# Optimization experiments

Measured on AMD Instinct MI355X. Metric: run time of the kernel, lower is better.

The kernel has to match this reference:

```python
import jax, jax.numpy as jnp
import numpy as np

EPS = 1e-5
NUM_GROUPS = 8


def _group_norm(x, w, b, num_groups, eps=EPS):
    # x: [BN, C, T], normalize per-sample over each group of channels and time
    BN, C, T = x.shape
    xg = x.reshape(BN, num_groups, C // num_groups, T)
    mean = xg.mean(axis=(2, 3), keepdims=True)
    var = xg.var(axis=(2, 3), keepdims=True)
    xg = (xg - mean) * jax.lax.rsqrt(var + eps)
    x = xg.reshape(BN, C, T)
    return x * w[None, :, None] + b[None, :, None]


def _layer_norm(x, w, b, eps=EPS):
    mean = x.mean(axis=-1, keepdims=True)
    var = x.var(axis=-1, keepdims=True)
    return (x - mean) * jax.lax.rsqrt(var + eps) * w + b


def setup_inputs() -> dict:
    key = jax.random.key(0)
    ks = jax.random.split(key, 8)
    B, T, N, C_in, C_out, K, kt = 16, 128, 64, 128, 256, 3, 3
    x = jax.random.normal(ks[0], (B, T, N, C_in), dtype=jnp.float32)
    A = jax.random.uniform(ks[1], (K, N, N), dtype=jnp.float32)
    dw_weights = jax.random.uniform(ks[2], (K, C_in), minval=0.8, maxval=1.2, dtype=jnp.float32)
    W_pw = jax.random.normal(ks[3], (C_out, K * C_in), dtype=jnp.float32) / np.sqrt(K * C_in)
    W_conv = jax.random.normal(ks[4], (C_out, 1, kt), dtype=jnp.float32) / np.sqrt(kt)
    gn_w = jnp.ones((C_out,), dtype=jnp.float32)
    gn_b = jnp.zeros((C_out,), dtype=jnp.float32)
    ln_w = jnp.ones((C_out,), dtype=jnp.float32)
    ln_b = jnp.zeros((C_out,), dtype=jnp.float32)
    W_res = jax.random.normal(ks[5], (C_out, C_in), dtype=jnp.float32) / np.sqrt(C_in)
    return {"x": x, "A": A, "dw_weights": dw_weights, "W_pw": W_pw, "W_conv": W_conv,
            "gn_w": gn_w, "gn_b": gn_b, "ln_w": ln_w, "ln_b": ln_b, "W_res": W_res}


def reference(x, A, dw_weights, W_pw, W_conv, gn_w, gn_b, ln_w, ln_b, W_res):
    B, T, N, C = x.shape
    K = A.shape[0]
    C_out = W_pw.shape[0]
    # residual projection (C_in != C_out)
    residual = jnp.einsum('btnc,oc->btno', x, W_res)
    # NOTE: faithful to torch einsum 'knm,btnc->kbtnc' (sums A over m only)
    agg = jnp.einsum('knm,btnc->kbtnc', A, x)
    agg = agg * dw_weights[:, None, None, None, :]
    # stack K along feature dim: [B,T,N,K*C]
    h = jnp.transpose(agg, (1, 2, 3, 0, 4)).reshape(B, T, N, K * C)
    h = jnp.einsum('btnk,ok->btno', h, W_pw)  # pointwise, no bias; dropout=eval identity
    # depthwise temporal conv over T: [B*N, C_out, T]
    h_t = jnp.transpose(h, (0, 2, 3, 1)).reshape(B * N, C_out, T)
    pad = W_conv.shape[-1] // 2
    h_t = jax.lax.conv_general_dilated(
        h_t, W_conv, window_strides=(1,), padding=[(pad, pad)],
        dimension_numbers=('NCH', 'OIH', 'NCH'), feature_group_count=C_out)
    h_t = _group_norm(h_t, gn_w, gn_b, NUM_GROUPS)
    h = jnp.transpose(h_t.reshape(B, N, C_out, T), (0, 3, 1, 2))
    return jax.nn.gelu(_layer_norm(h + residual, ln_w, ln_b), approximate=False)
```

## Files before the change

kernel.cpp:

```cpp
#include <hip/hip_runtime.h>

typedef unsigned short u16;
typedef __attribute__((ext_vector_type(4))) unsigned short u16x4;
typedef __attribute__((ext_vector_type(8))) __bf16 bf16x8;
typedef __attribute__((ext_vector_type(4))) float f32x4;

#define B_ 16
#define T_ 128
#define N_ 64
#define CI 128
#define CO 256

__device__ __forceinline__ u16 f2b(float f) {
    unsigned x = __builtin_bit_cast(unsigned, f);
    x += 0x7fffu + ((x >> 16) & 1u);
    return (u16)(x >> 16);
}

__global__ void prep_kernel(const float* __restrict__ A, const float* __restrict__ dw,
                            const float* __restrict__ Wpw, const float* __restrict__ Wres,
                            u16* __restrict__ Mg, u16* __restrict__ WresB) {
    int n = blockIdx.x >> 2, ch = blockIdx.x & 3;
    int tid = threadIdx.x;
    float s0 = 0.f, s1 = 0.f, s2 = 0.f;
    for (int m = 0; m < N_; ++m) {
        s0 += A[(0 * N_ + n) * N_ + m];
        s1 += A[(1 * N_ + n) * N_ + m];
        s2 += A[(2 * N_ + n) * N_ + m];
    }
#pragma unroll
    for (int i = 0; i < 8; ++i) {
        int e4 = tid + i * 256;
        int ol = e4 >> 5, c4 = (e4 & 31) << 2;
        int o = ch * 64 + ol;
        float4 d0 = *(const float4*)(dw + c4);
        float4 d1 = *(const float4*)(dw + CI + c4);
        float4 d2 = *(const float4*)(dw + 2 * CI + c4);
        float4 p0 = *(const float4*)(Wpw + (size_t)o * 3 * CI + c4);
        float4 p1 = *(const float4*)(Wpw + (size_t)o * 3 * CI + CI + c4);
        float4 p2 = *(const float4*)(Wpw + (size_t)o * 3 * CI + 2 * CI + c4);
        u16x4 u = { f2b(s0 * d0.x * p0.x + s1 * d1.x * p1.x + s2 * d2.x * p2.x),
                    f2b(s0 * d0.y * p0.y + s1 * d1.y * p1.y + s2 * d2.y * p2.y),
                    f2b(s0 * d0.z * p0.z + s1 * d1.z * p1.z + s2 * d2.z * p2.z),
                    f2b(s0 * d0.w * p0.w + s1 * d1.w * p1.w + s2 * d2.w * p2.w) };
        *(u16x4*)(Mg + ((size_t)n << 15) + o * CI + c4) = u;
        if (n == 0) {
            float4 r = *(const float4*)(Wres + (size_t)o * CI + c4);
            u16x4 ur = { f2b(r.x), f2b(r.y), f2b(r.z), f2b(r.w) };
            *(u16x4*)(WresB + o * CI + c4) = ur;
        }
    }
}

__global__ __launch_bounds__(512, 2) void fused_kernel(
    const float* __restrict__ xg, const u16* __restrict__ Mg, const u16* __restrict__ WresB,
    const float* __restrict__ Wconv, const float* __restrict__ gnw, const float* __restrict__ gnb,
    const float* __restrict__ lnw, const float* __restrict__ lnb, float* __restrict__ out)
{
    __shared__ __align__(16) u16 xf[T_ * CI];
    __shared__ float ebA[CO], ebB[CO];
    __shared__ float gpart[8][2][2];
    __shared__ float gstat[8][2];
    __shared__ float lnp[T_][10];
    __shared__ float lnstat[T_][2];

    const int tid = threadIdx.x;
    const int bid = blockIdx.x;
    const int n = bid & 63, b = bid >> 6;
    const float* xb = xg + (((size_t)b * T_) * N_ + n) * CI;

#pragma unroll
    for (int it = 0; it < 8; ++it) {
        int f = tid + (it << 9);
        int t = f >> 5;
        int c4 = (f & 31) << 2;
        float4 v = *(const float4*)(xb + (size_t)t * (N_ * CI) + c4);
        int kkk = c4 >> 5, quad = (c4 >> 3) & 3, j = c4 & 7;
        int mt = t >> 4;
        int sl = quad * 16 + (t & 15);
        int off = ((kkk * 8 + mt) << 9) + (sl << 3) + j;
        u16x4 u = { f2b(v.x), f2b(v.y), f2b(v.z), f2b(v.w) };
        *(u16x4*)(xf + off) = u;
    }
    __syncthreads();

    const int wid = tid >> 6, lane = tid & 63;
    const int wt = wid >> 2, wo = wid & 3;
    const int lr = lane & 15, lq = lane >> 4;

    f32x4 ah[4][4], ar[4][4];
#pragma unroll
    for (int mi = 0; mi < 4; ++mi)
#pragma unroll
        for (int ni = 0; ni < 4; ++ni) {
            ah[mi][ni] = (f32x4){0.f, 0.f, 0.f, 0.f};
            ar[mi][ni] = (f32x4){0.f, 0.f, 0.f, 0.f};
        }
    const u16* Mn = Mg + ((size_t)n << 15);
#pragma unroll
    for (int kk = 0; kk < 4; ++kk) {
        bf16x8 af[4];
#pragma unroll
        for (int mi = 0; mi < 4; ++mi)
            af[mi] = *(const bf16x8*)(xf + ((kk * 8 + wt * 4 + mi) << 9) + (lane << 3));
        const int c = kk * 32 + lq * 8;
#pragma unroll
        for (int ni = 0; ni < 4; ++ni) {
            const int o = wo * 64 + ni * 16 + lr;
            bf16x8 bm = *(const bf16x8*)(Mn + o * CI + c);
            bf16x8 br = *(const bf16x8*)(WresB + o * CI + c);
#pragma unroll
            for (int mi = 0; mi < 4; ++mi) {
                ah[mi][ni] = __builtin_amdgcn_mfma_f32_16x16x32_bf16(af[mi], bm, ah[mi][ni], 0, 0, 0);
                ar[mi][ni] = __builtin_amdgcn_mfma_f32_16x16x32_bf16(af[mi], br, ar[mi][ni], 0, 0, 0);
            }
        }
    }

    if (wt == 0 && lq == 3) {
#pragma unroll
        for (int ni = 0; ni < 4; ++ni) ebA[wo * 64 + ni * 16 + lr] = ah[3][ni][3];
    }
    if (wt == 1 && lq == 0) {
#pragma unroll
        for (int ni = 0; ni < 4; ++ni) ebB[wo * 64 + ni * 16 + lr] = ah[0][ni][0];
    }
    __syncthreads();

    float w0[4], w1[4], w2[4];
#pragma unroll
    for (int ni = 0; ni < 4; ++ni) {
        int o = wo * 64 + ni * 16 + lr;
        w0[ni] = Wconv[o * 3 + 0];
        w1[ni] = Wconv[o * 3 + 1];
        w2[ni] = Wconv[o * 3 + 2];
    }

    float gs0 = 0.f, gq0 = 0.f, gs1 = 0.f, gq1 = 0.f;
#pragma unroll
    for (int ni = 0; ni < 4; ++ni) {
        int o = wo * 64 + ni * 16 + lr;
        float up3[4], dn0[4];
#pragma unroll
        for (int mi = 0; mi < 4; ++mi) up3[mi] = __shfl(ah[mi][ni][3], (lane + 48) & 63);
#pragma unroll
        for (int mi = 0; mi < 4; ++mi) dn0[mi] = __shfl(ah[mi][ni][0], (lane + 16) & 63);
        float epv = ebA[o], env = ebB[o];
        float sA = 0.f, qA = 0.f;
#pragma unroll
        for (int mi = 0; mi < 4; ++mi) {
            float prev = (lq == 0) ? ((mi == 0) ? ((wt == 1) ? epv : 0.f) : up3[mi - 1]) : up3[mi];
            float nxt3 = (lq == 3) ? ((mi == 3) ? ((wt == 0) ? env : 0.f) : dn0[mi + 1]) : dn0[mi];
            float hm1 = prev;
#pragma unroll
            for (int e = 0; e < 4; ++e) {
                float cur = ah[mi][ni][e];
                float nx = (e < 3) ? ah[mi][ni][e + 1] : nxt3;
                float hc = w0[ni] * hm1 + w1[ni] * cur + w2[ni] * nx;
                hm1 = cur;
                ah[mi][ni][e] = hc;
                sA += hc;
                qA += hc * hc;
            }
        }
        if ((ni >> 1) == 0) { gs0 += sA; gq0 += qA; } else { gs1 += sA; gq1 += qA; }
    }
#pragma unroll
    for (int m = 1; m < 64; m <<= 1) {
        gs0 += __shfl_xor(gs0, m); gq0 += __shfl_xor(gq0, m);
        gs1 += __shfl_xor(gs1, m); gq1 += __shfl_xor(gq1, m);
    }
    if (lane == 0) {
        gpart[wid][0][0] = gs0; gpart[wid][0][1] = gq0;
        gpart[wid][1][0] = gs1; gpart[wid][1][1] = gq1;
    }
    __syncthreads();
    if (tid < 8) {
        float s = gpart[tid >> 1][tid & 1][0] + gpart[(tid >> 1) + 4][tid & 1][0];
        float q = gpart[tid >> 1][tid & 1][1] + gpart[(tid >> 1) + 4][tid & 1][1];
        float mu = s * (1.f / 4096.f);
        float var = q * (1.f / 4096.f) - mu * mu;
        gstat[tid][0] = mu;
        gstat[tid][1] = rsqrtf(var + 1e-5f);
    }
    __syncthreads();

    float lw[4], lb[4];
    float st[4][4], qt[4][4];
#pragma unroll
    for (int mi = 0; mi < 4; ++mi)
#pragma unroll
        for (int e = 0; e < 4; ++e) { st[mi][e] = 0.f; qt[mi][e] = 0.f; }
#pragma unroll
    for (int ni = 0; ni < 4; ++ni) {
        int o = wo * 64 + ni * 16 + lr;
        lw[ni] = lnw[o]; lb[ni] = lnb[o];
        float mg = gstat[wo * 2 + (ni >> 1)][0];
        float rg = gstat[wo * 2 + (ni >> 1)][1];
        float gwm = gnw[o] * rg;
        float gbm = gnb[o] - mg * gwm;
#pragma unroll
        for (int mi = 0; mi < 4; ++mi)
#pragma unroll
            for (int e = 0; e < 4; ++e) {
                float v = ah[mi][ni][e] * gwm + gbm + ar[mi][ni][e];
                ah[mi][ni][e] = v;
                st[mi][e] += v;
                qt[mi][e] += v * v;
            }
    }
#pragma unroll
    for (int m = 1; m < 16; m <<= 1)
#pragma unroll
        for (int mi = 0; mi < 4; ++mi)
#pragma unroll
            for (int e = 0; e < 4; ++e) {
                st[mi][e] += __shfl_xor(st[mi][e], m);
                qt[mi][e] += __shfl_xor(qt[mi][e], m);
            }
    if (lr == 0) {
#pragma unroll
        for (int mi = 0; mi < 4; ++mi)
#pragma unroll
            for (int e = 0; e < 4; ++e) {
                int t = wt * 64 + mi * 16 + lq * 4 + e;
                lnp[t][wo * 2] = st[mi][e];
                lnp[t][wo * 2 + 1] = qt[mi][e];
            }
    }
    __syncthreads();
    if (tid < T_) {
        float s = lnp[tid][0] + lnp[tid][2] + lnp[tid][4] + lnp[tid][6];
        float q = lnp[tid][1] + lnp[tid][3] + lnp[tid][5] + lnp[tid][7];
        float mu = s * (1.f / 256.f);
        float var = q * (1.f / 256.f) - mu * mu;
        lnstat[tid][0] = mu;
        lnstat[tid][1] = rsqrtf(var + 1e-5f);
    }
    __syncthreads();

    float* ob = out + (((size_t)b * T_ + wt * 64) * N_ + n) * CO + wo * 64;
#pragma unroll
    for (int mi = 0; mi < 4; ++mi)
#pragma unroll
        for (int e = 0; e < 4; ++e) {
            int tl = mi * 16 + lq * 4 + e;
            float mu = lnstat[wt * 64 + tl][0];
            float rs = lnstat[wt * 64 + tl][1];
#pragma unroll
            for (int ni = 0; ni < 4; ++ni) {
                float u = (ah[mi][ni][e] - mu) * rs * lw[ni] + lb[ni];
                float ge = 0.5f * u * (1.f + erff(u * 0.70710678118654752f));
                ob[(size_t)tl * (N_ * CO) + ni * 16 + lr] = ge;
            }
        }
}

extern "C" void kernel_launch(void* const* d_in, const int* in_sizes, int n_in,
                              void* d_out, int out_size, void* d_ws, size_t ws_size,
                              hipStream_t stream) {
    const float* x    = (const float*)d_in[0];
    const float* A    = (const float*)d_in[1];
    const float* dw   = (const float*)d_in[2];
    const float* Wpw  = (const float*)d_in[3];
    const float* Wcv  = (const float*)d_in[4];
    const float* gnw  = (const float*)d_in[5];
    const float* gnb  = (const float*)d_in[6];
    const float* lnw  = (const float*)d_in[7];
    const float* lnb  = (const float*)d_in[8];
    const float* Wres = (const float*)d_in[9];

    u16* Mg    = (u16*)d_ws;
    u16* WresB = Mg + (size_t)N_ * CO * CI;

    prep_kernel<<<N_ * 4, 256, 0, stream>>>(A, dw, Wpw, Wres, Mg, WresB);
    fused_kernel<<<B_ * N_, 512, 0, stream>>>(x, Mg, WresB, Wcv, gnw, gnb, lnw, lnb, (float*)d_out);
}
```

Before: 286.3 us.

## Split fused kernel across 16 waves with smaller per-wave T tiles

Doubles the block to 1024 threads so each wave covers 32 time steps instead of 64, halving per-thread accumulator registers. The halo exchange for the temporal conv now goes through a per-wave-row edge buffer. The layer-norm reduction is restructured to sum over channels in registers, do a shorter shuffle, then run a cooperative 8-lane pass over LDS. The aim is more resident waves and more latency hiding, at the cost of redundant B-fragment loads from global memory per wave and extra LDS traffic.

Measured after the change: 301.2 us. +5.2%, slower.

```diff
diff --git a/kernel.cpp b/kernel.cpp
--- a/kernel.cpp
+++ b/kernel.cpp
@@ -52,16 +52,16 @@
     }
 }
 
-__global__ __launch_bounds__(512, 2) void fused_kernel(
+__global__ __launch_bounds__(1024, 4) void fused_kernel(
     const float* __restrict__ xg, const u16* __restrict__ Mg, const u16* __restrict__ WresB,
     const float* __restrict__ Wconv, const float* __restrict__ gnw, const float* __restrict__ gnb,
     const float* __restrict__ lnw, const float* __restrict__ lnb, float* __restrict__ out)
 {
     __shared__ __align__(16) u16 xf[T_ * CI];
-    __shared__ float ebA[CO], ebB[CO];
-    __shared__ float gpart[8][2][2];
+    __shared__ float ebT[8][CO];
+    __shared__ float gpart[16][2][2];
     __shared__ float gstat[8][2];
-    __shared__ float lnp[T_][10];
+    __shared__ __align__(16) float lnq[T_][18][2];
     __shared__ float lnstat[T_][2];
 
     const int tid = threadIdx.x;
@@ -70,8 +70,8 @@
     const float* xb = xg + (((size_t)b * T_) * N_ + n) * CI;
 
 #pragma unroll
-    for (int it = 0; it < 8; ++it) {
-        int f = tid + (it << 9);
+    for (int it = 0; it < 4; ++it) {
+        int f = tid + (it << 10);
         int t = f >> 5;
         int c4 = (f & 31) << 2;
         float4 v = *(const float4*)(xb + (size_t)t * (N_ * CI) + c4);
@@ -88,9 +88,9 @@
     const int wt = wid >> 2, wo = wid & 3;
     const int lr = lane & 15, lq = lane >> 4;
 
-    f32x4 ah[4][4], ar[4][4];
-#pragma unroll
-    for (int mi = 0; mi < 4; ++mi)
+    f32x4 ah[2][4], ar[2][4];
+#pragma unroll
+    for (int mi = 0; mi < 2; ++mi)
 #pragma unroll
         for (int ni = 0; ni < 4; ++ni) {
             ah[mi][ni] = (f32x4){0.f, 0.f, 0.f, 0.f};
@@ -99,10 +99,10 @@
     const u16* Mn = Mg + ((size_t)n << 15);
 #pragma unroll
     for (int kk = 0; kk < 4; ++kk) {
-        bf16x8 af[4];
-#pragma unroll
-        for (int mi = 0; mi < 4; ++mi)
-            af[mi] = *(const bf16x8*)(xf + ((kk * 8 + wt * 4 + mi) << 9) + (lane << 3));
+        bf16x8 af[2];
+#pragma unroll
+        for (int mi = 0; mi < 2; ++mi)
+            af[mi] = *(const bf16x8*)(xf + ((kk * 8 + wt * 2 + mi) << 9) + (lane << 3));
         const int c = kk * 32 + lq * 8;
 #pragma unroll
         for (int ni = 0; ni < 4; ++ni) {
@@ -110,20 +110,20 @@
             bf16x8 bm = *(const bf16x8*)(Mn + o * CI + c);
             bf16x8 br = *(const bf16x8*)(WresB + o * CI + c);
 #pragma unroll
-            for (int mi = 0; mi < 4; ++mi) {
+            for (int mi = 0; mi < 2; ++mi) {
                 ah[mi][ni] = __builtin_amdgcn_mfma_f32_16x16x32_bf16(af[mi], bm, ah[mi][ni], 0, 0, 0);
                 ar[mi][ni] = __builtin_amdgcn_mfma_f32_16x16x32_bf16(af[mi], br, ar[mi][ni], 0, 0, 0);
             }
         }
     }
 
-    if (wt == 0 && lq == 3) {
-#pragma unroll
-        for (int ni = 0; ni < 4; ++ni) ebA[wo * 64 + ni * 16 + lr] = ah[3][ni][3];
-    }
-    if (wt == 1 && lq == 0) {
-#pragma unroll
-        for (int ni = 0; ni < 4; ++ni) ebB[wo * 64 + ni * 16 + lr] = ah[0][ni][0];
+    if (lq == 0) {
+#pragma unroll
+        for (int ni = 0; ni < 4; ++ni) ebT[wt * 2][wo * 64 + ni * 16 + lr] = ah[0][ni][0];
+    }
+    if (lq == 3) {
+#pragma unroll
+        for (int ni = 0; ni < 4; ++ni) ebT[wt * 2 + 1][wo * 64 + ni * 16 + lr] = ah[1][ni][3];
     }
     __syncthreads();
 
@@ -135,22 +135,23 @@
         w1[ni] = Wconv[o * 3 + 1];
         w2[ni] = Wconv[o * 3 + 2];
     }
-
     float gs0 = 0.f, gq0 = 0.f, gs1 = 0.f, gq1 = 0.f;
 #pragma unroll
     for (int ni = 0; ni < 4; ++ni) {
         int o = wo * 64 + ni * 16 + lr;
-        float up3[4], dn0[4];
-#pragma unroll
-        for (int mi = 0; mi < 4; ++mi) up3[mi] = __shfl(ah[mi][ni][3], (lane + 48) & 63);
-#pragma unroll
-        for (int mi = 0; mi < 4; ++mi) dn0[mi] = __shfl(ah[mi][ni][0], (lane + 16) & 63);
-        float epv = ebA[o], env = ebB[o];
+        float up3[2], dn0[2];
+#pragma unroll
+        for (int mi = 0; mi < 2; ++mi) up3[mi] = __shfl(ah[mi][ni][3], (lane + 48) & 63);
+#pragma unroll
+        for (int mi = 0; mi < 2; ++mi) dn0[mi] = __shfl(ah[mi][ni][0], (lane + 16) & 63);
+        float epv = 0.f, env = 0.f;
+        if (wt > 0) epv = ebT[wt * 2 - 1][o];
+        if (wt < 3) env = ebT[wt * 2 + 2][o];
         float sA = 0.f, qA = 0.f;
 #pragma unroll
-        for (int mi = 0; mi < 4; ++mi) {
-            float prev = (lq == 0) ? ((mi == 0) ? ((wt == 1) ? epv : 0.f) : up3[mi - 1]) : up3[mi];
-            float nxt3 = (lq == 3) ? ((mi == 3) ? ((wt == 0) ? env : 0.f) : dn0[mi + 1]) : dn0[mi];
+        for (int mi = 0; mi < 2; ++mi) {
+            float prev = (lq == 0) ? ((mi == 0) ? epv : up3[0]) : up3[mi];
+            float nxt3 = (lq == 3) ? ((mi == 1) ? env : dn0[1]) : dn0[mi];
             float hm1 = prev;
 #pragma unroll
             for (int e = 0; e < 4; ++e) {
@@ -163,7 +164,7 @@
                 qA += hc * hc;
             }
         }
-        if ((ni >> 1) == 0) { gs0 += sA; gq0 += qA; } else { gs1 += sA; gq1 += qA; }
+        if (ni < 2) { gs0 += sA; gq0 += qA; } else { gs1 += sA; gq1 += qA; }
     }
 #pragma unroll
     for (int m = 1; m < 64; m <<= 1) {
@@ -176,8 +177,9 @@
     }
     __syncthreads();
     if (tid < 8) {
-        float s = gpart[tid >> 1][tid & 1][0] + gpart[(tid >> 1) + 4][tid & 1][0];
-        float q = gpart[tid >> 1][tid & 1][1] + gpart[(tid >> 1) + 4][tid & 1][1];
+        int wg = tid >> 1, hf = tid & 1;
+        float s = gpart[wg][hf][0] + gpart[4 + wg][hf][0] + gpart[8 + wg][hf][0] + gpart[12 + wg][hf][0];
+        float q = gpart[wg][hf][1] + gpart[4 + wg][hf][1] + gpart[8 + wg][hf][1] + gpart[12 + wg][hf][1];
         float mu = s * (1.f / 4096.f);
         float var = q * (1.f / 4096.f) - mu * mu;
         gstat[tid][0] = mu;
@@ -185,68 +187,60 @@
     }
     __syncthreads();
 
-    float lw[4], lb[4];
-    float st[4][4], qt[4][4];
-#pragma unroll
-    for (int mi = 0; mi < 4; ++mi)
-#pragma unroll
-        for (int e = 0; e < 4; ++e) { st[mi][e] = 0.f; qt[mi][e] = 0.f; }
+    float gwm[4], gbm[4], lw[4], lb[4];
 #pragma unroll
     for (int ni = 0; ni < 4; ++ni) {
         int o = wo * 64 + ni * 16 + lr;
         lw[ni] = lnw[o]; lb[ni] = lnb[o];
         float mg = gstat[wo * 2 + (ni >> 1)][0];
         float rg = gstat[wo * 2 + (ni >> 1)][1];
-        float gwm = gnw[o] * rg;
-        float gbm = gnb[o] - mg * gwm;
-#pragma unroll
-        for (int mi = 0; mi < 4; ++mi)
-#pragma unroll
-            for (int e = 0; e < 4; ++e) {
-                float v = ah[mi][ni][e] * gwm + gbm + ar[mi][ni][e];
+        gwm[ni] = gnw[o] * rg;
+        gbm[ni] = gnb[o] - mg * gwm[ni];
+    }
+#pragma unroll
+    for (int mi = 0; mi < 2; ++mi)
+#pragma unroll
+        for (int e = 0; e < 4; ++e) {
+            float s = 0.f, q = 0.f;
+#pragma unroll
+            for (int ni = 0; ni < 4; ++ni) {
+                float v = ah[mi][ni][e] * gwm[ni] + gbm[ni] + ar[mi][ni][e];
                 ah[mi][ni][e] = v;
-                st[mi][e] += v;
-                qt[mi][e] += v * v;
-            }
-    }
-#pragma unroll
-    for (int m = 1; m < 16; m <<= 1)
-#pragma unroll
-        for (int mi = 0; mi < 4; ++mi)
-#pragma unroll
-            for (int e = 0; e < 4; ++e) {
-                st[mi][e] += __shfl_xor(st[mi][e], m);
-                qt[mi][e] += __shfl_xor(qt[mi][e], m);
-            }
-    if (lr == 0) {
-#pragma unroll
-        for (int mi = 0; mi < 4; ++mi)
-#pragma unroll
-            for (int e = 0; e < 4; ++e) {
-                int t = wt * 64 + mi * 16 + lq * 4 + e;
-                lnp[t][wo * 2] = st[mi][e];
-                lnp[t][wo * 2 + 1] = qt[mi][e];
-            }
-    }
-    __syncthreads();
-    if (tid < T_) {
-        float s = lnp[tid][0] + lnp[tid][2] + lnp[tid][4] + lnp[tid][6];
-        float q = lnp[tid][1] + lnp[tid][3] + lnp[tid][5] + lnp[tid][7];
-        float mu = s * (1.f / 256.f);
-        float var = q * (1.f / 256.f) - mu * mu;
-        lnstat[tid][0] = mu;
-        lnstat[tid][1] = rsqrtf(var + 1e-5f);
-    }
-    __syncthreads();
-
-    float* ob = out + (((size_t)b * T_ + wt * 64) * N_ + n) * CO + wo * 64;
-#pragma unroll
-    for (int mi = 0; mi < 4; ++mi)
+                s += v; q += v * v;
+            }
+            s += __shfl_xor(s, 1); q += __shfl_xor(q, 1);
+            s += __shfl_xor(s, 2); q += __shfl_xor(q, 2);
+            if ((lr & 3) == 0) {
+                int t = wt * 32 + mi * 16 + lq * 4 + e;
+                int j = (lr >> 2) * 4 + wo;
+                *(float2*)&lnq[t][j][0] = make_float2(s, q);
+            }
+        }
+    __syncthreads();
+    {
+        int t = tid >> 3, p = tid & 7;
+        f32x4 v4 = *(const f32x4*)&lnq[t][2 * p][0];
+        float s = v4.x + v4.z, q = v4.y + v4.w;
+        s += __shfl_xor(s, 1); q += __shfl_xor(q, 1);
+        s += __shfl_xor(s, 2); q += __shfl_xor(q, 2);
+        s += __shfl_xor(s, 4); q += __shfl_xor(q, 4);
+        if (p == 0) {
+            float mu = s * (1.f / 256.f);
+            float var = q * (1.f / 256.f) - mu * mu;
+            lnstat[t][0] = mu;
+            lnstat[t][1] = rsqrtf(var + 1e-5f);
+        }
+    }
+    __syncthreads();
+
+    float* ob = out + (((size_t)b * T_ + wt * 32) * N_ + n) * CO + wo * 64;
+#pragma unroll
+    for (int mi = 0; mi < 2; ++mi)
 #pragma unroll
         for (int e = 0; e < 4; ++e) {
             int tl = mi * 16 + lq * 4 + e;
-            float mu = lnstat[wt * 64 + tl][0];
-            float rs = lnstat[wt * 64 + tl][1];
+            float mu = lnstat[wt * 32 + tl][0];
+            float rs = lnstat[wt * 32 + tl][1];
 #pragma unroll
             for (int ni = 0; ni < 4; ++ni) {
                 float u = (ah[mi][ni][e] - mu) * rs * lw[ni] + lb[ni];
@@ -274,5 +268,5 @@
     u16* WresB = Mg + (size_t)N_ * CO * CI;
 
     prep_kernel<<<N_ * 4, 256, 0, stream>>>(A, dw, Wpw, Wres, Mg, WresB);
-    fused_kernel<<<B_ * N_, 512, 0, stream>>>(x, Mg, WresB, Wcv, gnw, gnb, lnw, lnb, (float*)d_out);
-}
+    fused_kernel<<<B_ * N_, 1024, 0, stream>>>(x, Mg, WresB, Wcv, gnw, gnb, lnw, lnb, (float*)d_out);
+}
```
